# Kernel optimization log

Measured on AMD Instinct MI355X. Metric: run time of the kernel, lower is better.

## Reference

```python
import jax, jax.numpy as jnp
import numpy as np

D_MODEL = 1024
NHEAD = 16
D_HEAD = D_MODEL // NHEAD
D_FF = 4096
B, S = 2, 2048
EPS = 1e-5


def _linear_params(key, d_in, d_out):
    kw, kb = jax.random.split(key)
    bound = 1.0 / np.sqrt(d_in)
    W = jax.random.uniform(kw, (d_out, d_in), jnp.float32, -bound, bound)
    b = jax.random.uniform(kb, (d_out,), jnp.float32, -bound, bound)
    return W, b


def setup_inputs() -> dict:
    key = jax.random.key(0)
    ks = jax.random.split(key, 8)
    x = jax.random.normal(ks[0], (B, S, D_MODEL), jnp.float32)
    Wq, bq = _linear_params(ks[1], D_MODEL, D_MODEL)
    Wk, bk = _linear_params(ks[2], D_MODEL, D_MODEL)
    Wv, bv = _linear_params(ks[3], D_MODEL, D_MODEL)
    Wo, bo = _linear_params(ks[4], D_MODEL, D_MODEL)
    W1, b1 = _linear_params(ks[5], D_MODEL, D_FF)
    W2, b2 = _linear_params(ks[6], D_FF, D_MODEL)
    g1 = jnp.ones((D_MODEL,), jnp.float32); be1 = jnp.zeros((D_MODEL,), jnp.float32)
    g2 = jnp.ones((D_MODEL,), jnp.float32); be2 = jnp.zeros((D_MODEL,), jnp.float32)
    return dict(x=x, Wq=Wq, bq=bq, Wk=Wk, bk=bk, Wv=Wv, bv=bv, Wo=Wo, bo=bo,
                W1=W1, b1=b1, W2=W2, b2=b2, g1=g1, be1=be1, g2=g2, be2=be2)


def _layernorm(x, g, b):
    mu = jnp.mean(x, axis=-1, keepdims=True)
    var = jnp.mean(jnp.square(x - mu), axis=-1, keepdims=True)
    return (x - mu) * jax.lax.rsqrt(var + EPS) * g + b


def reference(x, Wq, bq, Wk, bk, Wv, bv, Wo, bo, W1, b1, W2, b2, g1, be1, g2, be2):
    b_, s_, _ = x.shape
    # QKV projections (nn.Linear: x @ W.T + b)
    q = x @ Wq.T + bq
    k = x @ Wk.T + bk
    v = x @ Wv.T + bv
    # split heads -> [b, h, s, d_head]
    qh = q.reshape(b_, s_, NHEAD, D_HEAD).transpose(0, 2, 1, 3)
    kh = k.reshape(b_, s_, NHEAD, D_HEAD).transpose(0, 2, 1, 3)
    vh = v.reshape(b_, s_, NHEAD, D_HEAD).transpose(0, 2, 1, 3)
    scores = jnp.einsum('bhqd,bhkd->bhqk', qh, kh) / jnp.sqrt(jnp.float32(D_HEAD))
    attn_w = jax.nn.softmax(scores, axis=-1)
    attn_out = jnp.einsum('bhqk,bhkd->bhqd', attn_w, vh)
    attn_concat = attn_out.transpose(0, 2, 1, 3).reshape(b_, s_, D_MODEL)
    attn_proj = attn_concat @ Wo.T + bo
    # residual + LN1
    h = _layernorm(x + attn_proj, g1, be1)
    # FFN
    ffn = jax.nn.relu(h @ W1.T + b1) @ W2.T + b2
    # residual + LN2
    return _layernorm(h + ffn, g2, be2)
```

## Files before the change

kernel.cpp:

```cpp
#include <hip/hip_runtime.h>
#include <hip/hip_bf16.h>

#define D_MODEL 1024
#define NHEAD 16
#define D_HEAD 64
#define D_FF 4096
#define BATCH 2
#define SEQ 2048
#define M_TOK (BATCH * SEQ)
#define EPS 1e-5f
#define QKV_N 3072

using bf16 = __hip_bfloat16;
typedef __attribute__((ext_vector_type(8))) short short8;
typedef __attribute__((ext_vector_type(4))) float float4v;

__device__ __forceinline__ float b2f(unsigned short u) {
    union { unsigned int i; float f; } v; v.i = ((unsigned int)u) << 16; return v.f;
}
__device__ __forceinline__ unsigned short f2b(float f) {
    union { float f; unsigned int u; } v; v.f = f;
    unsigned int r = v.u + 0x7FFFu + ((v.u >> 16) & 1u);
    return (unsigned short)(r >> 16);
}
__device__ __forceinline__ float loadAt(const void* p, size_t i, int f32) {
    if (f32) return ((const float*)p)[i];
    return b2f(((const unsigned short*)p)[i]);
}
__device__ __forceinline__ void async16(const void* g, void* lds) {
    __builtin_amdgcn_global_load_lds(
        (const __attribute__((address_space(1))) unsigned int*)g,
        (__attribute__((address_space(3))) unsigned int*)lds, 16, 0, 0);
}

__global__ void detect_kernel(const unsigned short* __restrict__ x, int* __restrict__ flag) {
    __shared__ int cnt;
    if (threadIdx.x == 0) cnt = 0;
    __syncthreads();
    int c = 0;
    for (int i = threadIdx.x; i < 8192; i += 256) {
        unsigned short u = x[i];
        int e = (u >> 7) & 0xFF;
        if (e >= 0xF0) c++;
    }
    atomicAdd(&cnt, c);
    __syncthreads();
    if (threadIdx.x == 0) { flag[0] = (cnt > 16) ? 1 : 0; flag[1] = 0; }
}

__global__ __launch_bounds__(256) void cast_bf16_kernel(
    const void* __restrict__ src, bf16* __restrict__ dst, int n,
    const int* __restrict__ flagp) {
    const int f32 = *flagp;
    int i0 = (blockIdx.x * 256 + threadIdx.x) * 8;
    if (i0 >= n) return;
    short8 v;
    if (f32) {
        const float* pf = (const float*)src + i0;
        float4v f0 = *(const float4v*)pf;
        float4v f1 = *(const float4v*)(pf + 4);
#pragma unroll
        for (int i = 0; i < 4; i++) { v[i] = (short)f2b(f0[i]); v[4 + i] = (short)f2b(f1[i]); }
    } else {
        v = *(const short8*)((const short*)src + i0);
    }
    *(short8*)((short*)dst + i0) = v;
}

__global__ __launch_bounds__(256) void cast3_bf16_kernel(
    const void* __restrict__ s0, const void* __restrict__ s1,
    const void* __restrict__ s2, bf16* __restrict__ dst,
    const int* __restrict__ flagp) {
    const int f32 = *flagp;
    int i0 = (blockIdx.x * 256 + threadIdx.x) * 8;
    const int part = i0 >> 20;
    const int off = i0 & ((1 << 20) - 1);
    const void* src = (part == 0) ? s0 : (part == 1) ? s1 : s2;
    short8 v;
    if (f32) {
        const float* pf = (const float*)src + off;
        float4v f0 = *(const float4v*)pf;
        float4v f1 = *(const float4v*)(pf + 4);
#pragma unroll
        for (int i = 0; i < 4; i++) { v[i] = (short)f2b(f0[i]); v[4 + i] = (short)f2b(f1[i]); }
    } else {
        v = *(const short8*)((const short*)src + off);
    }
    *(short8*)((short*)dst + i0) = v;
}

__global__ __launch_bounds__(256) void cast2_bf16_kernel(
    const void* __restrict__ s0, const void* __restrict__ s1,
    bf16* __restrict__ d0, bf16* __restrict__ d1,
    const int* __restrict__ flagp) {
    const int f32 = *flagp;
    int i0 = (blockIdx.x * 256 + threadIdx.x) * 8;
    const void* src; short* dst; int off;
    if (i0 < (1 << 20)) { src = s0; dst = (short*)d0; off = i0; }
    else                { src = s1; dst = (short*)d1; off = i0 - (1 << 20); }
    short8 v;
    if (f32) {
        const float* pf = (const float*)src + off;
        float4v f0 = *(const float4v*)pf;
        float4v f1 = *(const float4v*)(pf + 4);
#pragma unroll
        for (int i = 0; i < 4; i++) { v[i] = (short)f2b(f0[i]); v[4 + i] = (short)f2b(f1[i]); }
    } else {
        v = *(const short8*)((const short*)src + off);
    }
    *(short8*)(dst + off) = v;
}

__device__ __forceinline__ void stage8(const void* src, size_t off, int f32, short* dst) {
    short8 v;
    if (f32) {
        const float* pf = (const float*)src + off;
        float4v f0 = *(const float4v*)pf;
        float4v f1 = *(const float4v*)(pf + 4);
#pragma unroll
        for (int i = 0; i < 4; i++) { v[i] = (short)f2b(f0[i]); v[4 + i] = (short)f2b(f1[i]); }
    } else {
        v = *(const short8*)((const short*)src + off);
    }
    *(short8*)dst = v;
}

template <int MF, int NF, bool RELU, bool BDYN>
__global__ __launch_bounds__(256) void gemm_mfma(
    const bf16* __restrict__ A, const void* __restrict__ B,
    const void* __restrict__ bias0, const void* __restrict__ bias1,
    const void* __restrict__ bias2, int nb1, int nb2,
    bf16* __restrict__ C, int N, int K, const int* __restrict__ inFlagp) {
    constexpr int BM = 32 * MF, BN = 32 * NF;
    __shared__ short As[BM * 64];
    __shared__ short Bs[BN * 64];
    const int tid = threadIdx.x;
    const int lane = tid & 63;
    const int wv = tid >> 6;
    const int wm = wv & 1, wn = wv >> 1;
    const int quad = lane >> 4, lrow = lane & 15;
    const int rowM = blockIdx.y * BM;
    const int rowN = blockIdx.x * BN;
    const int inf = *inFlagp;

    float4v acc[MF][NF];
    const float4v zero = {0.f, 0.f, 0.f, 0.f};
#pragma unroll
    for (int i = 0; i < MF; i++)
#pragma unroll
        for (int j = 0; j < NF; j++) acc[i][j] = zero;

    const int sRow = lane >> 3;
    const int gChunk = (lane & 7) ^ sRow;

    for (int k0 = 0; k0 < K; k0 += 64) {
#pragma unroll
        for (int rd = 0; rd < MF; rd++) {
            const short* gp = (const short*)A +
                (size_t)(rowM + rd * 32 + wv * 8 + sRow) * K + k0 + gChunk * 8;
            async16(gp, &As[rd * 2048 + wv * 512]);
        }
        if (!BDYN) {
#pragma unroll
            for (int rd = 0; rd < NF; rd++) {
                const short* gp = (const short*)B +
                    (size_t)(rowN + rd * 32 + wv * 8 + sRow) * K + k0 + gChunk * 8;
                async16(gp, &Bs[rd * 2048 + wv * 512]);
            }
        } else {
            const int brow = tid >> 2;
            const int c0 = (tid & 3) * 2;
#pragma unroll
            for (int cc = 0; cc < 2; cc++) {
                int slot = c0 + cc;
                int g = slot ^ (brow & 7);
                stage8(B, (size_t)(rowN + brow) * K + k0 + g * 8, inf,
                       &Bs[brow * 64 + slot * 8]);
            }
        }
        __syncthreads();
#pragma unroll
        for (int ks = 0; ks < 2; ks++) {
            short8 a_frag[MF], b_frag[NF];
#pragma unroll
            for (int i = 0; i < MF; i++) {
                const int row = wm * MF * 16 + i * 16 + lrow;
                const int slot = (ks * 4 + quad) ^ (row & 7);
                a_frag[i] = *(const short8*)&As[row * 64 + slot * 8];
            }
#pragma unroll
            for (int j = 0; j < NF; j++) {
                const int row = wn * NF * 16 + j * 16 + lrow;
                const int slot = (ks * 4 + quad) ^ (row & 7);
                b_frag[j] = *(const short8*)&Bs[row * 64 + slot * 8];
            }
#pragma unroll
            for (int i = 0; i < MF; i++)
#pragma unroll
                for (int j = 0; j < NF; j++)
                    acc[i][j] = __builtin_amdgcn_mfma_f32_16x16x32_bf16(
                        a_frag[i], b_frag[j], acc[i][j], 0, 0, 0);
        }
        __syncthreads();
    }

    const int mB = rowM + wm * MF * 16, nB = rowN + wn * NF * 16;
    unsigned short* Cu = (unsigned short*)C;
#pragma unroll
    for (int j = 0; j < NF; j++) {
        const int col = nB + j * 16 + lrow;
        float bv;
        if (col < nb1)      bv = loadAt(bias0, col, inf);
        else if (col < nb2) bv = loadAt(bias1, col - nb1, inf);
        else                bv = loadAt(bias2, col - nb2, inf);
#pragma unroll
        for (int i = 0; i < MF; i++) {
#pragma unroll
            for (int r = 0; r < 4; r++) {
                const int rowg = mB + i * 16 + quad * 4 + r;
                float vv = acc[i][j][r] + bv;
                if (RELU) vv = fmaxf(vv, 0.0f);
                Cu[(size_t)rowg * N + col] = f2b(vv);
            }
        }
    }
}

#define ASTRIDE 68
__global__ __launch_bounds__(512) void flash_attn_kernel(
    const bf16* __restrict__ Qb, const bf16* __restrict__ Kb,
    const bf16* __restrict__ Vb, bf16* __restrict__ O) {
    const int bid = blockIdx.x;
    const int qt = bid & 15;
    const int h  = (bid >> 4) & 15;
    const int b  = bid >> 8;
    const int q0 = qt * 128;
    const int tid = threadIdx.x;
    const int lane = tid & 63;
    const int wv = tid >> 6;
    const int quad = lane >> 4, lrow = lane & 15;

    __shared__ short Ps[128 * ASTRIDE];
    __shared__ short Ks[64 * 64];
    __shared__ short Vt[64 * ASTRIDE];

    const size_t headOff = (size_t)h * D_HEAD;
    const float SCF = 0.18033688f;

    {
        int r = tid >> 2, c0 = (tid & 3) * 16;
        const short* src = (const short*)Qb + (size_t)(b * SEQ + q0 + r) * QKV_N + headOff + c0;
#pragma unroll
        for (int half = 0; half < 2; half++) {
            short8 v = *(const short8*)(src + half * 8);
            short8 o;
#pragma unroll
            for (int e = 0; e < 8; e++)
                o[e] = (short)f2b(b2f((unsigned short)v[e]) * SCF);
            *(short8*)&Ps[r * ASTRIDE + c0 + half * 8] = o;
        }
    }
    __syncthreads();
    short8 a_q[2];
    a_q[0] = *(const short8*)&Ps[(wv * 16 + lrow) * ASTRIDE + 0 * 32 + quad * 8];
    a_q[1] = *(const short8*)&Ps[(wv * 16 + lrow) * ASTRIDE + 1 * 32 + quad * 8];

    float4v o_acc[4];
    const float4v zero = {0.f, 0.f, 0.f, 0.f};
#pragma unroll
    for (int dt = 0; dt < 4; dt++) o_acc[dt] = zero;
    float lsum[4] = {0.f, 0.f, 0.f, 0.f};

    const int sRow = lane >> 3;
    const int gChunk = (lane & 7) ^ sRow;

    for (int j0 = 0; j0 < SEQ; j0 += 64) {
        __syncthreads();
        {
            const short* gp = (const short*)Kb +
                (size_t)(b * SEQ + j0 + wv * 8 + sRow) * QKV_N + headOff + gChunk * 8;
            async16(gp, &Ks[wv * 512]);
        }
        {
            int jp = (tid & 31) * 2, d0 = (tid >> 5) * 4;
            const short* s0 = (const short*)Vb + (size_t)(b * SEQ + j0 + jp) * QKV_N + headOff + d0;
            const short* s1 = s0 + QKV_N;
#pragma unroll
            for (int e = 0; e < 4; e++) {
                unsigned int w = (unsigned int)*(const unsigned short*)(s0 + e) |
                                 ((unsigned int)*(const unsigned short*)(s1 + e) << 16);
                *(unsigned int*)&Vt[(d0 + e) * ASTRIDE + jp] = w;
            }
        }
        __syncthreads();

        float4v s_acc[4];
#pragma unroll
        for (int jn = 0; jn < 4; jn++) s_acc[jn] = zero;
#pragma unroll
        for (int ks = 0; ks < 2; ks++)
#pragma unroll
            for (int jn = 0; jn < 4; jn++) {
                const int row = jn * 16 + lrow;
                const int slot = (ks * 4 + quad) ^ (row & 7);
                short8 bfr = *(const short8*)&Ks[row * 64 + slot * 8];
                s_acc[jn] = __builtin_amdgcn_mfma_f32_16x16x32_bf16(a_q[ks], bfr, s_acc[jn], 0, 0, 0);
            }

        float p[4][4];
#pragma unroll
        for (int r = 0; r < 4; r++) {
            float ls = 0.f;
#pragma unroll
            for (int jn = 0; jn < 4; jn++) {
                float pv = exp2f(s_acc[jn][r]);
                p[jn][r] = pv;
                ls += pv;
            }
            lsum[r] += ls;
        }

#pragma unroll
        for (int jn = 0; jn < 4; jn++)
#pragma unroll
            for (int r = 0; r < 4; r++)
                Ps[(wv * 16 + quad * 4 + r) * ASTRIDE + jn * 16 + lrow] = (short)f2b(p[jn][r]);
        __syncthreads();

#pragma unroll
        for (int ks = 0; ks < 2; ks++) {
            short8 pa = *(const short8*)&Ps[(wv * 16 + lrow) * ASTRIDE + ks * 32 + quad * 8];
#pragma unroll
            for (int dt = 0; dt < 4; dt++) {
                short8 vb = *(const short8*)&Vt[(dt * 16 + lrow) * ASTRIDE + ks * 32 + quad * 8];
                o_acc[dt] = __builtin_amdgcn_mfma_f32_16x16x32_bf16(pa, vb, o_acc[dt], 0, 0, 0);
            }
        }
    }

    float invl[4];
#pragma unroll
    for (int r = 0; r < 4; r++) {
        float t = lsum[r];
        t += __shfl_xor(t, 1);
        t += __shfl_xor(t, 2);
        t += __shfl_xor(t, 4);
        t += __shfl_xor(t, 8);
        invl[r] = 1.0f / t;
    }
    unsigned short* Ou = (unsigned short*)O;
#pragma unroll
    for (int dt = 0; dt < 4; dt++)
#pragma unroll
        for (int r = 0; r < 4; r++) {
            const int rowg = b * SEQ + q0 + wv * 16 + quad * 4 + r;
            Ou[(size_t)rowg * D_MODEL + headOff + dt * 16 + lrow] = f2b(o_acc[dt][r] * invl[r]);
        }
}

template <bool OUT_F32>
__global__ __launch_bounds__(256) void add_ln_kernel(
    const void* __restrict__ X, const bf16* __restrict__ R,
    const void* __restrict__ g, const void* __restrict__ be,
    void* __restrict__ Y,
    const int* __restrict__ xFlagp, const int* __restrict__ wFlagp) {
    const int xf = *xFlagp;
    const int wf = *wFlagp;
    const int row = blockIdx.x;
    const size_t base = (size_t)row * D_MODEL;
    const int tid = threadIdx.x;
    __shared__ float red[256];
    float v[4];
#pragma unroll
    for (int i = 0; i < 4; i++) {
        int idx = tid + i * 256;
        v[i] = loadAt(X, base + idx, xf) + __bfloat162float(R[base + idx]);
    }
    float s = v[0] + v[1] + v[2] + v[3];
    red[tid] = s; __syncthreads();
    for (int s2 = 128; s2 > 0; s2 >>= 1) {
        if (tid < s2) red[tid] += red[tid + s2];
        __syncthreads();
    }
    float mu = red[0] * (1.0f / D_MODEL);
    __syncthreads();
    float s2v = 0.f;
#pragma unroll
    for (int i = 0; i < 4; i++) { float dd = v[i] - mu; s2v += dd * dd; }
    red[tid] = s2v; __syncthreads();
    for (int s2 = 128; s2 > 0; s2 >>= 1) {
        if (tid < s2) red[tid] += red[tid + s2];
        __syncthreads();
    }
    float rstd = rsqrtf(red[0] * (1.0f / D_MODEL) + EPS);
    __syncthreads();
#pragma unroll
    for (int i = 0; i < 4; i++) {
        int idx = tid + i * 256;
        float o = (v[i] - mu) * rstd * loadAt(g, idx, wf) + loadAt(be, idx, wf);
        if (OUT_F32) ((float*)Y)[base + idx] = o;
        else         ((bf16*)Y)[base + idx] = __float2bfloat16(o);
    }
}

extern "C" void kernel_launch(void* const* d_in, const int* in_sizes, int n_in,
                              void* d_out, int out_size, void* d_ws, size_t ws_size,
                              hipStream_t stream) {
    const void* x  = d_in[0];
    const void* Wq = d_in[1];  const void* bq = d_in[2];
    const void* Wk = d_in[3];  const void* bk = d_in[4];
    const void* Wv = d_in[5];  const void* bv = d_in[6];
    const void* Wo = d_in[7];  const void* bo = d_in[8];
    const void* W1 = d_in[9];  const void* b1 = d_in[10];
    const void* W2 = d_in[11]; const void* b2 = d_in[12];
    const void* g1 = d_in[13]; const void* be1 = d_in[14];
    const void* g2 = d_in[15]; const void* be2 = d_in[16];

    char* ws = (char*)d_ws;
    const size_t MB = 1024 * 1024;
    bf16* xb     = (bf16*)(ws + 0 * MB);
    bf16* wqkvb  = (bf16*)(ws + 8 * MB);
    bf16* wob    = (bf16*)(ws + 14 * MB);
    bf16* qkv    = (bf16*)(ws + 16 * MB);
    bf16* concat = (bf16*)(ws + 40 * MB);
    bf16* w1b    = (bf16*)(ws + 0 * MB);
    bf16* proj   = (bf16*)(ws + 16 * MB);
    bf16* hb     = (bf16*)(ws + 8 * MB);
    bf16* ffn1   = (bf16*)(ws + 16 * MB);
    bf16* ffn2   = (bf16*)(ws + 0 * MB);
    const bool castW2 = (ws_size >= 56 * MB + 8);
    bf16* w2b    = (bf16*)(ws + 48 * MB);
    int*  flag   = (int*)(ws + (castW2 ? 56 * MB : 48 * MB));

    const int* fIn = flag;
    const int* fBf = flag + 1;

    dim3 blk(256);

    detect_kernel<<<dim3(1), blk, 0, stream>>>((const unsigned short*)x, flag);
    cast_bf16_kernel<<<dim3((M_TOK * D_MODEL / 8 + 255) / 256), blk, 0, stream>>>(x, xb, M_TOK * D_MODEL, fIn);
    cast3_bf16_kernel<<<dim3(3 * D_MODEL * D_MODEL / 8 / 256), blk, 0, stream>>>(Wq, Wk, Wv, wqkvb, fIn);
    if (castW2)
        cast_bf16_kernel<<<dim3((D_FF * D_MODEL / 8 + 255) / 256), blk, 0, stream>>>(W2, w2b, D_FF * D_MODEL, fIn);
    gemm_mfma<4, 4, false, false><<<dim3(QKV_N / 128, M_TOK / 128), blk, 0, stream>>>(
        xb, wqkvb, bq, bk, bv, 1024, 2048, qkv, QKV_N, D_MODEL, fIn);
    cast2_bf16_kernel<<<dim3(5 * D_MODEL * D_MODEL / 8 / 256), blk, 0, stream>>>(Wo, W1, wob, w1b, fIn);
    flash_attn_kernel<<<dim3(BATCH * NHEAD * (SEQ / 128)), dim3(512), 0, stream>>>(
        qkv, qkv + D_MODEL, qkv + 2 * D_MODEL, concat);
    gemm_mfma<2, 2, false, false><<<dim3(D_MODEL / 64, M_TOK / 64), blk, 0, stream>>>(
        concat, wob, bo, bo, bo, D_MODEL, D_MODEL, proj, D_MODEL, D_MODEL, fIn);
    add_ln_kernel<false><<<dim3(M_TOK), blk, 0, stream>>>(x, proj, g1, be1, hb, fIn, fIn);
    gemm_mfma<4, 4, true, false><<<dim3(D_FF / 128, M_TOK / 128), blk, 0, stream>>>(
        hb, w1b, b1, b1, b1, D_FF, D_FF, ffn1, D_FF, D_MODEL, fIn);
    if (castW2)
        gemm_mfma<2, 2, false, false><<<dim3(D_MODEL / 64, M_TOK / 64), blk, 0, stream>>>(
            ffn1, w2b, b2, b2, b2, D_MODEL, D_MODEL, ffn2, D_MODEL, D_FF, fIn);
    else
        gemm_mfma<2, 2, false, true><<<dim3(D_MODEL / 64, M_TOK / 64), blk, 0, stream>>>(
            ffn1, W2, b2, b2, b2, D_MODEL, D_MODEL, ffn2, D_MODEL, D_FF, fIn);
    add_ln_kernel<true><<<dim3(M_TOK), blk, 0, stream>>>(hb, ffn2, g2, be2, d_out, fBf, fIn);
}
```

Before: 405.0 us.

## Switch flash attention to 32x32 MFMA tiles and vectorize add-layernorm

The attention kernel moves from eight waves using 16x16x32 MFMA to four waves using 32x32x16 MFMA. Each wave now owns 32 query rows, and the V tile is loaded with wider vector loads. Because each wave only touches its own P rows, the block barrier between writing P and reading it is removed, and P is converted to bf16 by truncation instead of rounding. The add+layernorm kernel now uses contiguous 4-element vector loads and stores. Risks: the 66-element LDS row stride makes the 16-byte LDS reads misaligned, and truncating P costs some precision.

Result: no change. 405.1 us (+0.0%).

```diff
diff --git a/kernel.cpp b/kernel.cpp
--- a/kernel.cpp
+++ b/kernel.cpp
@@ -13,7 +13,9 @@
 
 using bf16 = __hip_bfloat16;
 typedef __attribute__((ext_vector_type(8))) short short8;
+typedef __attribute__((ext_vector_type(4))) short short4v;
 typedef __attribute__((ext_vector_type(4))) float float4v;
+typedef __attribute__((ext_vector_type(16))) float float16v;
 
 __device__ __forceinline__ float b2f(unsigned short u) {
     union { unsigned int i; float f; } v; v.i = ((unsigned int)u) << 16; return v.f;
@@ -226,8 +228,8 @@
     }
 }
 
-#define ASTRIDE 68
-__global__ __launch_bounds__(512) void flash_attn_kernel(
+#define FSTRIDE 66
+__global__ __launch_bounds__(256) void flash_attn_kernel(
     const bf16* __restrict__ Qb, const bf16* __restrict__ Kb,
     const bf16* __restrict__ Vb, bf16* __restrict__ O) {
     const int bid = blockIdx.x;
@@ -238,123 +240,120 @@
     const int tid = threadIdx.x;
     const int lane = tid & 63;
     const int wv = tid >> 6;
-    const int quad = lane >> 4, lrow = lane & 15;
-
-    __shared__ short Ps[128 * ASTRIDE];
+    const int half = lane >> 5;
+    const int l31 = lane & 31;
+
+    __shared__ short Ps[128 * FSTRIDE];
     __shared__ short Ks[64 * 64];
-    __shared__ short Vt[64 * ASTRIDE];
+    __shared__ short Vt[64 * FSTRIDE];
 
     const size_t headOff = (size_t)h * D_HEAD;
     const float SCF = 0.18033688f;
 
     {
-        int r = tid >> 2, c0 = (tid & 3) * 16;
+        int r = tid >> 1, c0 = (tid & 1) * 32;
         const short* src = (const short*)Qb + (size_t)(b * SEQ + q0 + r) * QKV_N + headOff + c0;
 #pragma unroll
-        for (int half = 0; half < 2; half++) {
-            short8 v = *(const short8*)(src + half * 8);
+        for (int ch = 0; ch < 4; ch++) {
+            short8 v = *(const short8*)(src + ch * 8);
             short8 o;
 #pragma unroll
             for (int e = 0; e < 8; e++)
                 o[e] = (short)f2b(b2f((unsigned short)v[e]) * SCF);
-            *(short8*)&Ps[r * ASTRIDE + c0 + half * 8] = o;
+            *(short8*)&Ps[r * FSTRIDE + c0 + ch * 8] = o;
         }
     }
     __syncthreads();
-    short8 a_q[2];
-    a_q[0] = *(const short8*)&Ps[(wv * 16 + lrow) * ASTRIDE + 0 * 32 + quad * 8];
-    a_q[1] = *(const short8*)&Ps[(wv * 16 + lrow) * ASTRIDE + 1 * 32 + quad * 8];
-
-    float4v o_acc[4];
-    const float4v zero = {0.f, 0.f, 0.f, 0.f};
-#pragma unroll
-    for (int dt = 0; dt < 4; dt++) o_acc[dt] = zero;
-    float lsum[4] = {0.f, 0.f, 0.f, 0.f};
+    short8 a_q[4];
+#pragma unroll
+    for (int ks = 0; ks < 4; ks++)
+        a_q[ks] = *(const short8*)&Ps[(wv * 32 + l31) * FSTRIDE + ks * 16 + half * 8];
+
+    float16v o_acc[2];
+    float lsum[16];
+#pragma unroll
+    for (int i = 0; i < 16; i++) { o_acc[0][i] = 0.f; o_acc[1][i] = 0.f; lsum[i] = 0.f; }
 
     const int sRow = lane >> 3;
     const int gChunk = (lane & 7) ^ sRow;
 
     for (int j0 = 0; j0 < SEQ; j0 += 64) {
         __syncthreads();
+#pragma unroll
+        for (int rd = 0; rd < 2; rd++) {
+            const short* gp = (const short*)Kb +
+                (size_t)(b * SEQ + j0 + wv * 16 + rd * 8 + sRow) * QKV_N + headOff + gChunk * 8;
+            async16(gp, &Ks[(wv * 16 + rd * 8) * 64]);
+        }
         {
-            const short* gp = (const short*)Kb +
-                (size_t)(b * SEQ + j0 + wv * 8 + sRow) * QKV_N + headOff + gChunk * 8;
-            async16(gp, &Ks[wv * 512]);
-        }
-        {
-            int jp = (tid & 31) * 2, d0 = (tid >> 5) * 4;
+            int jp = (tid & 31) * 2, d0 = (tid >> 5) * 8;
             const short* s0 = (const short*)Vb + (size_t)(b * SEQ + j0 + jp) * QKV_N + headOff + d0;
-            const short* s1 = s0 + QKV_N;
-#pragma unroll
-            for (int e = 0; e < 4; e++) {
-                unsigned int w = (unsigned int)*(const unsigned short*)(s0 + e) |
-                                 ((unsigned int)*(const unsigned short*)(s1 + e) << 16);
-                *(unsigned int*)&Vt[(d0 + e) * ASTRIDE + jp] = w;
-            }
-        }
-        __syncthreads();
-
-        float4v s_acc[4];
-#pragma unroll
-        for (int jn = 0; jn < 4; jn++) s_acc[jn] = zero;
-#pragma unroll
-        for (int ks = 0; ks < 2; ks++)
-#pragma unroll
-            for (int jn = 0; jn < 4; jn++) {
-                const int row = jn * 16 + lrow;
-                const int slot = (ks * 4 + quad) ^ (row & 7);
+            short8 v0 = *(const short8*)s0;
+            short8 v1 = *(const short8*)(s0 + QKV_N);
+#pragma unroll
+            for (int e = 0; e < 8; e++) {
+                unsigned int w = (unsigned int)(unsigned short)v0[e] |
+                                 ((unsigned int)(unsigned short)v1[e] << 16);
+                *(unsigned int*)&Vt[(d0 + e) * FSTRIDE + jp] = w;
+            }
+        }
+        __syncthreads();
+
+        float16v s_acc[2];
+#pragma unroll
+        for (int i = 0; i < 16; i++) { s_acc[0][i] = 0.f; s_acc[1][i] = 0.f; }
+#pragma unroll
+        for (int ks = 0; ks < 4; ks++)
+#pragma unroll
+            for (int jb = 0; jb < 2; jb++) {
+                const int row = jb * 32 + l31;
+                const int slot = (ks * 2 + half) ^ (l31 & 7);
                 short8 bfr = *(const short8*)&Ks[row * 64 + slot * 8];
-                s_acc[jn] = __builtin_amdgcn_mfma_f32_16x16x32_bf16(a_q[ks], bfr, s_acc[jn], 0, 0, 0);
-            }
-
-        float p[4][4];
-#pragma unroll
-        for (int r = 0; r < 4; r++) {
-            float ls = 0.f;
-#pragma unroll
-            for (int jn = 0; jn < 4; jn++) {
-                float pv = exp2f(s_acc[jn][r]);
-                p[jn][r] = pv;
-                ls += pv;
-            }
-            lsum[r] += ls;
-        }
-
-#pragma unroll
-        for (int jn = 0; jn < 4; jn++)
-#pragma unroll
-            for (int r = 0; r < 4; r++)
-                Ps[(wv * 16 + quad * 4 + r) * ASTRIDE + jn * 16 + lrow] = (short)f2b(p[jn][r]);
-        __syncthreads();
-
-#pragma unroll
-        for (int ks = 0; ks < 2; ks++) {
-            short8 pa = *(const short8*)&Ps[(wv * 16 + lrow) * ASTRIDE + ks * 32 + quad * 8];
-#pragma unroll
-            for (int dt = 0; dt < 4; dt++) {
-                short8 vb = *(const short8*)&Vt[(dt * 16 + lrow) * ASTRIDE + ks * 32 + quad * 8];
-                o_acc[dt] = __builtin_amdgcn_mfma_f32_16x16x32_bf16(pa, vb, o_acc[dt], 0, 0, 0);
-            }
-        }
-    }
-
-    float invl[4];
-#pragma unroll
-    for (int r = 0; r < 4; r++) {
-        float t = lsum[r];
+                s_acc[jb] = __builtin_amdgcn_mfma_f32_32x32x16_bf16(a_q[ks], bfr, s_acc[jb], 0, 0, 0);
+            }
+
+#pragma unroll
+        for (int jb = 0; jb < 2; jb++)
+#pragma unroll
+            for (int reg = 0; reg < 16; reg++) {
+                float pv = exp2f(s_acc[jb][reg]);
+                lsum[reg] += pv;
+                union { float f; unsigned int u; } uu; uu.f = pv;
+                const int rowC = (reg & 3) + 8 * (reg >> 2) + 4 * half;
+                Ps[(wv * 32 + rowC) * FSTRIDE + jb * 32 + l31] = (short)(uu.u >> 16);
+            }
+
+#pragma unroll
+        for (int ks = 0; ks < 4; ks++) {
+            short8 pa = *(const short8*)&Ps[(wv * 32 + l31) * FSTRIDE + ks * 16 + half * 8];
+#pragma unroll
+            for (int db = 0; db < 2; db++) {
+                short8 vb = *(const short8*)&Vt[(db * 32 + l31) * FSTRIDE + ks * 16 + half * 8];
+                o_acc[db] = __builtin_amdgcn_mfma_f32_32x32x16_bf16(pa, vb, o_acc[db], 0, 0, 0);
+            }
+        }
+    }
+
+    float invl[16];
+#pragma unroll
+    for (int reg = 0; reg < 16; reg++) {
+        float t = lsum[reg];
         t += __shfl_xor(t, 1);
         t += __shfl_xor(t, 2);
         t += __shfl_xor(t, 4);
         t += __shfl_xor(t, 8);
-        invl[r] = 1.0f / t;
+        t += __shfl_xor(t, 16);
+        invl[reg] = 1.0f / t;
     }
     unsigned short* Ou = (unsigned short*)O;
 #pragma unroll
-    for (int dt = 0; dt < 4; dt++)
-#pragma unroll
-        for (int r = 0; r < 4; r++) {
-            const int rowg = b * SEQ + q0 + wv * 16 + quad * 4 + r;
-            Ou[(size_t)rowg * D_MODEL + headOff + dt * 16 + lrow] = f2b(o_acc[dt][r] * invl[r]);
+    for (int db = 0; db < 2; db++)
+#pragma unroll
+        for (int reg = 0; reg < 16; reg++) {
+            const int rowC = (reg & 3) + 8 * (reg >> 2) + 4 * half;
+            const int rowg = b * SEQ + q0 + wv * 32 + rowC;
+            Ou[(size_t)rowg * D_MODEL + headOff + db * 32 + l31] =
+                f2b(o_acc[db][reg] * invl[reg]);
         }
 }
 
@@ -369,12 +368,19 @@
     const int row = blockIdx.x;
     const size_t base = (size_t)row * D_MODEL;
     const int tid = threadIdx.x;
+    const int i0 = tid * 4;
     __shared__ float red[256];
     float v[4];
-#pragma unroll
-    for (int i = 0; i < 4; i++) {
-        int idx = tid + i * 256;
-        v[i] = loadAt(X, base + idx, xf) + __bfloat162float(R[base + idx]);
+    if (xf) {
+        float4v xv = *(const float4v*)((const float*)X + base + i0);
+        short4v rv = *(const short4v*)((const short*)R + base + i0);
+#pragma unroll
+        for (int i = 0; i < 4; i++) v[i] = xv[i] + b2f((unsigned short)rv[i]);
+    } else {
+        short4v xv = *(const short4v*)((const short*)X + base + i0);
+        short4v rv = *(const short4v*)((const short*)R + base + i0);
+#pragma unroll
+        for (int i = 0; i < 4; i++) v[i] = b2f((unsigned short)xv[i]) + b2f((unsigned short)rv[i]);
     }
     float s = v[0] + v[1] + v[2] + v[3];
     red[tid] = s; __syncthreads();
@@ -393,13 +399,28 @@
         __syncthreads();
     }
     float rstd = rsqrtf(red[0] * (1.0f / D_MODEL) + EPS);
-    __syncthreads();
-#pragma unroll
-    for (int i = 0; i < 4; i++) {
-        int idx = tid + i * 256;
-        float o = (v[i] - mu) * rstd * loadAt(g, idx, wf) + loadAt(be, idx, wf);
-        if (OUT_F32) ((float*)Y)[base + idx] = o;
-        else         ((bf16*)Y)[base + idx] = __float2bfloat16(o);
+    float gv[4], bv[4];
+    if (wf) {
+        float4v gg = *(const float4v*)((const float*)g + i0);
+        float4v bb = *(const float4v*)((const float*)be + i0);
+#pragma unroll
+        for (int i = 0; i < 4; i++) { gv[i] = gg[i]; bv[i] = bb[i]; }
+    } else {
+        short4v gg = *(const short4v*)((const short*)g + i0);
+        short4v bb = *(const short4v*)((const short*)be + i0);
+#pragma unroll
+        for (int i = 0; i < 4; i++) { gv[i] = b2f((unsigned short)gg[i]); bv[i] = b2f((unsigned short)bb[i]); }
+    }
+    if (OUT_F32) {
+        float4v o;
+#pragma unroll
+        for (int i = 0; i < 4; i++) o[i] = (v[i] - mu) * rstd * gv[i] + bv[i];
+        *(float4v*)((float*)Y + base + i0) = o;
+    } else {
+        short4v o;
+#pragma unroll
+        for (int i = 0; i < 4; i++) o[i] = (short)f2b((v[i] - mu) * rstd * gv[i] + bv[i]);
+        *(short4v*)((short*)Y + base + i0) = o;
     }
 }
 
@@ -445,7 +466,7 @@
     gemm_mfma<4, 4, false, false><<<dim3(QKV_N / 128, M_TOK / 128), blk, 0, stream>>>(
         xb, wqkvb, bq, bk, bv, 1024, 2048, qkv, QKV_N, D_MODEL, fIn);
     cast2_bf16_kernel<<<dim3(5 * D_MODEL * D_MODEL / 8 / 256), blk, 0, stream>>>(Wo, W1, wob, w1b, fIn);
-    flash_attn_kernel<<<dim3(BATCH * NHEAD * (SEQ / 128)), dim3(512), 0, stream>>>(
+    flash_attn_kernel<<<dim3(BATCH * NHEAD * (SEQ / 128)), blk, 0, stream>>>(
         qkv, qkv + D_MODEL, qkv + 2 * D_MODEL, concat);
     gemm_mfma<2, 2, false, false><<<dim3(D_MODEL / 64, M_TOK / 64), blk, 0, stream>>>(
         concat, wob, bo, bo, bo, D_MODEL, D_MODEL, proj, D_MODEL, D_MODEL, fIn);
```
